# Kernel optimization log

Hardware: AMD Instinct MI355X
Metric: run time of the kernel (lower is better)

Reference implementation:

```python
import jax, jax.numpy as jnp
import numpy as np

B, T, E, H = 256, 1024, 32, 128
N_OBS = 1048576
N_OBS_VOCAB = 11  # n_lands + 2
N_ACT_VOCAB = 5   # n_acts + 2


def setup_inputs() -> dict:
    key = jax.random.key(0)
    ks = jax.random.split(key, 10)
    obs_ids = jax.random.randint(ks[0], (N_OBS,), 0, N_OBS_VOCAB)
    obs_slot = jnp.sort(jax.random.randint(ks[1], (N_OBS,), 0, B * T))
    action_ids = jax.random.randint(ks[2], (B, T), 0, N_ACT_VOCAB)
    is_action = jax.random.bernoulli(ks[3], 0.5, (B, T))
    lengths = jax.random.randint(ks[4], (B,), T // 4, T + 1)
    input_lengths = jnp.sort(lengths)[::-1]  # pack_padded_sequence requires descending
    s = 1.0 / np.sqrt(H)
    action_emb = jax.random.normal(ks[5], (N_ACT_VOCAB, E), jnp.float32)
    obs_emb = jax.random.normal(ks[6], (N_OBS_VOCAB, E), jnp.float32)
    W_ih = jax.random.uniform(ks[7], (4 * H, E), jnp.float32, -s, s)
    W_hh = jax.random.uniform(ks[8], (4 * H, H), jnp.float32, -s, s)
    b_ih = jax.random.uniform(ks[9], (4 * H,), jnp.float32, -s, s)
    b_hh = jnp.zeros((4 * H,), jnp.float32)
    return dict(obs_ids=obs_ids, obs_slot=obs_slot, action_ids=action_ids,
                is_action=is_action, input_lengths=input_lengths,
                action_emb=action_emb, obs_emb=obs_emb,
                W_ih=W_ih, W_hh=W_hh, b_ih=b_ih, b_hh=b_hh)


def _embed(obs_ids, obs_slot, action_ids, is_action, action_emb, obs_emb):
    # fused ragged embedding-bag: gather + segment-sum over observation lists
    obs_sum = jax.ops.segment_sum(obs_emb[obs_ids], obs_slot, num_segments=B * T)
    obs_sum = obs_sum.reshape(B, T, E)
    act = action_emb[action_ids]  # [B,T,E]
    return jnp.where(is_action[..., None], act, obs_sum)


def _lstm(embedded, input_lengths, W_ih, W_hh, b_ih, b_hh):
    mask = (jnp.arange(T)[None, :] < input_lengths[:, None])  # [B,T]
    xs = jnp.swapaxes(embedded, 0, 1)                         # [T,B,E]
    ms = mask.T[..., None].astype(embedded.dtype)             # [T,B,1]

    def step(carry, inp):
        h, c = carry
        x, m = inp
        gates = x @ W_ih.T + h @ W_hh.T + (b_ih + b_hh)  # [B,4H]
        i, f, g, o = jnp.split(gates, 4, axis=-1)        # torch gate order i,f,g,o
        i, f, o = jax.nn.sigmoid(i), jax.nn.sigmoid(f), jax.nn.sigmoid(o)
        g = jnp.tanh(g)
        c_new = f * c + i * g
        h_new = o * jnp.tanh(c_new)
        h = m * h_new + (1.0 - m) * h  # frozen past length (packed semantics)
        c = m * c_new + (1.0 - m) * c
        return (h, c), h * m           # pad_packed zero-pads past length

    h0 = jnp.zeros((B, H), embedded.dtype)
    c0 = jnp.zeros((B, H), embedded.dtype)
    (hN, cN), outs = jax.lax.scan(step, (h0, c0), (xs, ms))
    return jnp.swapaxes(outs, 0, 1), hN[None], cN[None]  # outputs [B,T,H], h/c [1,B,H]


def reference(obs_ids, obs_slot, action_ids, is_action, input_lengths,
              action_emb, obs_emb, W_ih, W_hh, b_ih, b_hh):
    embedded = _embed(obs_ids, obs_slot, action_ids, is_action, action_emb, obs_emb)
    outputs, h, c = _lstm(embedded, input_lengths, W_ih, W_hh, b_ih, b_hh)
    return outputs, h, c, embedded
```

## Files before the change

### kernel.cpp

```cpp
#include <hip/hip_runtime.h>

#define B_ 256
#define T_ 1024
#define E_ 32
#define H_ 128
#define NOBS_ 1048576
#define RPB 4
#define NBLK (B_ / RPB)
#define NW 8
#define THREADS (NW * 64)

#define HROW 144
#define HBUF (RPB * HROW)

#define L2E 1.4426950408889634f

typedef __attribute__((ext_vector_type(8))) short bf16x8;
typedef __attribute__((ext_vector_type(4))) float f32x4;
typedef __attribute__((ext_vector_type(4))) int   i32x4;

#define LDS_BARRIER() asm volatile("s_waitcnt lgkmcnt(0)\n\ts_barrier" ::: "memory")

__device__ __forceinline__ short f2bf(float x) {
    unsigned u = __float_as_uint(x);
    unsigned r = u + 0x7FFFu + ((u >> 16) & 1u);
    return (short)(r >> 16);
}

__global__ void embed_kernel(const int* __restrict__ obs_ids,
                             const int* __restrict__ obs_slot,
                             const int* __restrict__ action_ids,
                             const int* __restrict__ is_action,
                             const float* __restrict__ action_emb,
                             const float* __restrict__ obs_emb,
                             float* __restrict__ embedded) {
    __shared__ float s_act[5 * E_];
    __shared__ float s_obs[11 * E_];
    for (int i = threadIdx.x; i < 5 * E_; i += blockDim.x) s_act[i] = action_emb[i];
    for (int i = threadIdx.x; i < 11 * E_; i += blockDim.x) s_obs[i] = obs_emb[i];
    __syncthreads();

    int s = blockIdx.x * blockDim.x + threadIdx.x;
    if (s >= B_ * T_) return;

    float acc[E_];
    if (is_action[s]) {
        int a = action_ids[s];
        #pragma unroll
        for (int e = 0; e < E_; e++) acc[e] = s_act[a * E_ + e];
    } else {
        #pragma unroll
        for (int e = 0; e < E_; e++) acc[e] = 0.0f;
        int lo = 0, hi = NOBS_;
        while (lo < hi) {
            int mid = (lo + hi) >> 1;
            if (obs_slot[mid] < s) lo = mid + 1; else hi = mid;
        }
        int j = lo;
        while (j < NOBS_ && obs_slot[j] == s) {
            int id = obs_ids[j];
            #pragma unroll
            for (int e = 0; e < E_; e++) acc[e] += s_obs[id * E_ + e];
            j++;
        }
    }
    float4* dst = (float4*)(embedded + (size_t)s * E_);
    #pragma unroll
    for (int q = 0; q < E_ / 4; q++) {
        float4 v; v.x = acc[4*q]; v.y = acc[4*q+1]; v.z = acc[4*q+2]; v.w = acc[4*q+3];
        dst[q] = v;
    }
}

__launch_bounds__(THREADS, 2)
__global__ void lstm_kernel(const float* __restrict__ embedded,
                            const int* __restrict__ lengths,
                            const float* __restrict__ W_ih,
                            const float* __restrict__ W_hh,
                            const float* __restrict__ b_ih,
                            const float* __restrict__ b_hh,
                            float* __restrict__ outputs,
                            float* __restrict__ h_out,
                            float* __restrict__ c_out) {
    __shared__ __align__(16) char h_lds[2 * HBUF];

    const int tid  = threadIdx.x;
    const int lane = tid & 63;
    const int wave = tid >> 6;
    const int row0 = blockIdx.x * RPB;

    const int col16  = (wave << 4) + (lane & 15);
    const int kgrp8  = (lane >> 4) * 8;
    const int kgrp16 = (lane >> 4) * 16;
    const int brow   = (lane & 15) >> 2;
    const int g_own  = lane >> 4;

    bf16x8 wx[4];
    f32x4  biasv[4];
    i32x4  wh[4][2];
    float  dq[4];
    #pragma unroll
    for (int gt = 0; gt < 4; gt++) {
        const float scale = (gt == 2) ? (2.0f * L2E) : L2E;
        const int gcol = gt * H_ + col16;
        {
            const float* p = W_ih + (size_t)gcol * E_ + kgrp8;
            bf16x8 v;
            #pragma unroll
            for (int j = 0; j < 8; j++) v[j] = f2bf(p[j] * scale);
            wx[gt] = v;
        }
        biasv[gt] = (f32x4)((b_ih[gcol] + b_hh[gcol]) * scale);

        const float* q = W_hh + (size_t)gcol * H_;
        float m = 0.0f;
        #pragma unroll
        for (int t2 = 0; t2 < 2; t2++)
            #pragma unroll
            for (int j = 0; j < 16; j++)
                m = fmaxf(m, fabsf(q[t2 * 64 + kgrp16 + j]));
        m = fmaxf(m, __shfl_xor(m, 16));
        m = fmaxf(m, __shfl_xor(m, 32));
        const float s = 127.0f / m;
        dq[gt] = scale * m * (1.0f / (127.0f * 127.0f));
        #pragma unroll
        for (int t2 = 0; t2 < 2; t2++) {
            i32x4 v;
            #pragma unroll
            for (int d = 0; d < 4; d++) {
                int word = 0;
                #pragma unroll
                for (int b2 = 0; b2 < 4; b2++) {
                    int qi = (int)rintf(q[t2 * 64 + kgrp16 + d * 4 + b2] * s);
                    word |= (qi & 0xFF) << (b2 * 8);
                }
                v[d] = word;
            }
            wh[gt][t2] = v;
        }
    }

    const int len = lengths[row0 + g_own];
    float cr = 0.0f, hr = 0.0f;

    const float* xp = embedded + ((size_t)(row0 + brow) * T_) * E_ + kgrp8;

    const int rbase = brow * HROW + kgrp16;
    const int wofs  = g_own * HROW + col16;
    float* const out_base = outputs + (size_t)(row0 + g_own) * T_ * H_ + col16;

    for (int i = tid; i < 2 * HBUF; i += THREADS) h_lds[i] = 0;
    __syncthreads();

    float4 xAlo = *(const float4*)(xp + 0 * E_);
    float4 xAhi = *(const float4*)(xp + 0 * E_ + 4);
    float4 xBlo = *(const float4*)(xp + 1 * E_);
    float4 xBhi = *(const float4*)(xp + 1 * E_ + 4);

    auto step = [&](int t, int RD, int WR, float4& xlo, float4& xhi, bool PF) {
        i32x4 ah0 = *(const i32x4*)&h_lds[RD + rbase + 0 * 64];
        i32x4 ah1 = *(const i32x4*)&h_lds[RD + rbase + 1 * 64];

        int x0, x1, x2, x3;
        asm("v_cvt_pk_bf16_f32 %0, %1, %2" : "=v"(x0) : "v"(xlo.x), "v"(xlo.y));
        asm("v_cvt_pk_bf16_f32 %0, %1, %2" : "=v"(x1) : "v"(xlo.z), "v"(xlo.w));
        asm("v_cvt_pk_bf16_f32 %0, %1, %2" : "=v"(x2) : "v"(xhi.x), "v"(xhi.y));
        asm("v_cvt_pk_bf16_f32 %0, %1, %2" : "=v"(x3) : "v"(xhi.z), "v"(xhi.w));
        i32x4 xi; xi[0] = x0; xi[1] = x1; xi[2] = x2; xi[3] = x3;
        bf16x8 xa = __builtin_bit_cast(bf16x8, xi);

        if (PF) {
            const float* xq = xp + (size_t)(t + 2) * E_;
            xlo = *(const float4*)(xq + 0);
            xhi = *(const float4*)(xq + 4);
        }

        f32x4 accf[4];
        i32x4 acci[4];
        const i32x4 zero = (i32x4)0;
        #pragma unroll
        for (int gt = 0; gt < 4; gt++)
            accf[gt] = __builtin_amdgcn_mfma_f32_16x16x32_bf16(xa, wx[gt], biasv[gt], 0, 0, 0);
        #pragma unroll
        for (int gt = 0; gt < 4; gt++)
            acci[gt] = __builtin_amdgcn_mfma_i32_16x16x64_i8(ah0, wh[gt][0], zero, 0, 0, 0);
        #pragma unroll
        for (int gt = 0; gt < 4; gt++)
            acci[gt] = __builtin_amdgcn_mfma_i32_16x16x64_i8(ah1, wh[gt][1], acci[gt], 0, 0, 0);

        float a_i = fmaf((float)acci[0][0], dq[0], accf[0][0]);
        float a_f = fmaf((float)acci[1][0], dq[1], accf[1][0]);
        float a_g = fmaf((float)acci[2][0], dq[2], accf[2][0]);
        float a_o = fmaf((float)acci[3][0], dq[3], accf[3][0]);

        float Ai = exp2f(-a_i);
        float Eg = exp2f(fminf(a_g, 80.0f));
        float ig = (Eg - 1.0f) * __builtin_amdgcn_rcpf((1.0f + Ai) * (Eg + 1.0f));
        float Af = exp2f(-a_f);
        float f_ = __builtin_amdgcn_rcpf(1.0f + Af);
        float c_new = fmaf(f_, cr, ig);
        float Ec = exp2f(fminf((2.0f * L2E) * c_new, 80.0f));
        float Ao = exp2f(-a_o);
        float h_new = (Ec - 1.0f) * __builtin_amdgcn_rcpf((1.0f + Ao) * (Ec + 1.0f));

        bool m = (t < len);
        cr = m ? c_new : cr;
        hr = m ? h_new : hr;
        out_base[(size_t)t * H_] = m ? h_new : 0.0f;

        int qh = (int)rintf(hr * 127.0f);
        h_lds[WR + wofs] = (char)qh;

        LDS_BARRIER();
    };

    for (int t = 0; t < T_ - 2; t += 2) {
        step(t,     0,    HBUF, xAlo, xAhi, true);
        step(t + 1, HBUF, 0,    xBlo, xBhi, true);
    }
    step(T_ - 2, 0,    HBUF, xAlo, xAhi, false);
    step(T_ - 1, HBUF, 0,    xBlo, xBhi, false);

    h_out[(size_t)(row0 + g_own) * H_ + col16] = hr;
    c_out[(size_t)(row0 + g_own) * H_ + col16] = cr;
}

extern "C" void kernel_launch(void* const* d_in, const int* in_sizes, int n_in,
                              void* d_out, int out_size, void* d_ws, size_t ws_size,
                              hipStream_t stream) {
    const int*   obs_ids       = (const int*)d_in[0];
    const int*   obs_slot      = (const int*)d_in[1];
    const int*   action_ids    = (const int*)d_in[2];
    const int*   is_action     = (const int*)d_in[3];
    const int*   input_lengths = (const int*)d_in[4];
    const float* action_emb    = (const float*)d_in[5];
    const float* obs_emb       = (const float*)d_in[6];
    const float* W_ih          = (const float*)d_in[7];
    const float* W_hh          = (const float*)d_in[8];
    const float* b_ih          = (const float*)d_in[9];
    const float* b_hh          = (const float*)d_in[10];

    float* out      = (float*)d_out;
    float* outputs  = out;
    float* h_out    = out + (size_t)B_ * T_ * H_;
    float* c_out    = h_out + (size_t)B_ * H_;
    float* embedded = c_out + (size_t)B_ * H_;

    hipLaunchKernelGGL(embed_kernel, dim3((B_ * T_ + 255) / 256), dim3(256), 0, stream,
                       obs_ids, obs_slot, action_ids, is_action, action_emb, obs_emb, embedded);

    hipLaunchKernelGGL(lstm_kernel, dim3(NBLK), dim3(THREADS), 0, stream,
                       embedded, input_lengths, W_ih, W_hh, b_ih, b_hh,
                       outputs, h_out, c_out);
}
```

Before: 487.9 us.

## Precompute bf16 inputs in embed kernel and software-pipeline input projection MFMAs

The embed kernel now also writes a bf16 copy of the embeddings into workspace when enough workspace is available, so the LSTM kernel loads one 16-byte vector per step instead of two float4 loads plus conversions. The input-projection MFMAs for step t+1 are issued after the recurrent MFMAs of step t, taking them off the serial h-dependency chain. The cost is an extra bf16 write in the embed kernel and more live accumulator registers, which could hurt occupancy; it falls back to the fp32 path if the workspace is too small.

```diff
diff --git a/kernel.cpp b/kernel.cpp
--- a/kernel.cpp
+++ b/kernel.cpp
@@ -33,7 +33,8 @@
                              const int* __restrict__ is_action,
                              const float* __restrict__ action_emb,
                              const float* __restrict__ obs_emb,
-                             float* __restrict__ embedded) {
+                             float* __restrict__ embedded,
+                             unsigned short* __restrict__ xbf) {
     __shared__ float s_act[5 * E_];
     __shared__ float s_obs[11 * E_];
     for (int i = threadIdx.x; i < 5 * E_; i += blockDim.x) s_act[i] = action_emb[i];
@@ -70,10 +71,20 @@
         float4 v; v.x = acc[4*q]; v.y = acc[4*q+1]; v.z = acc[4*q+2]; v.w = acc[4*q+3];
         dst[q] = v;
     }
+    if (xbf) {
+        unsigned short tmp[E_];
+        #pragma unroll
+        for (int e = 0; e < E_; e++) tmp[e] = (unsigned short)f2bf(acc[e]);
+        int4* d2 = (int4*)(xbf + (size_t)s * E_);
+        #pragma unroll
+        for (int q = 0; q < E_ / 8; q++) d2[q] = ((const int4*)tmp)[q];
+    }
 }
 
+template<bool BF16X>
 __launch_bounds__(THREADS, 2)
 __global__ void lstm_kernel(const float* __restrict__ embedded,
+                            const unsigned short* __restrict__ xbf,
                             const int* __restrict__ lengths,
                             const float* __restrict__ W_ih,
                             const float* __restrict__ W_hh,
@@ -143,7 +154,8 @@
     const int len = lengths[row0 + g_own];
     float cr = 0.0f, hr = 0.0f;
 
-    const float* xp = embedded + ((size_t)(row0 + brow) * T_) * E_ + kgrp8;
+    const unsigned short* xpb = xbf + ((size_t)(row0 + brow) * T_) * E_ + kgrp8;
+    const float*          xpf = embedded + ((size_t)(row0 + brow) * T_) * E_ + kgrp8;
 
     const int rbase = brow * HROW + kgrp16;
     const int wofs  = g_own * HROW + col16;
@@ -152,46 +164,69 @@
     for (int i = tid; i < 2 * HBUF; i += THREADS) h_lds[i] = 0;
     __syncthreads();
 
-    float4 xAlo = *(const float4*)(xp + 0 * E_);
-    float4 xAhi = *(const float4*)(xp + 0 * E_ + 4);
-    float4 xBlo = *(const float4*)(xp + 1 * E_);
-    float4 xBhi = *(const float4*)(xp + 1 * E_ + 4);
-
-    auto step = [&](int t, int RD, int WR, float4& xlo, float4& xhi, bool PF) {
+    int4 xfA, xfB;
+    float4 flA, fhA, flB, fhB;
+    auto loadx = [&](int t, int4& xi4, float4& fl, float4& fh) {
+        if (BF16X) {
+            xi4 = *(const int4*)(xpb + (size_t)t * E_);
+        } else {
+            fl = *(const float4*)(xpf + (size_t)t * E_);
+            fh = *(const float4*)(xpf + (size_t)t * E_ + 4);
+        }
+    };
+    auto mkfrag = [&](const int4& xi4, const float4& fl, const float4& fh) -> bf16x8 {
+        if (BF16X) {
+            return __builtin_bit_cast(bf16x8, xi4);
+        } else {
+            int x0, x1, x2, x3;
+            asm("v_cvt_pk_bf16_f32 %0, %1, %2" : "=v"(x0) : "v"(fl.x), "v"(fl.y));
+            asm("v_cvt_pk_bf16_f32 %0, %1, %2" : "=v"(x1) : "v"(fl.z), "v"(fl.w));
+            asm("v_cvt_pk_bf16_f32 %0, %1, %2" : "=v"(x2) : "v"(fh.x), "v"(fh.y));
+            asm("v_cvt_pk_bf16_f32 %0, %1, %2" : "=v"(x3) : "v"(fh.z), "v"(fh.w));
+            i32x4 xi; xi[0] = x0; xi[1] = x1; xi[2] = x2; xi[3] = x3;
+            return __builtin_bit_cast(bf16x8, xi);
+        }
+    };
+
+    loadx(0, xfA, flA, fhA);
+    loadx(1, xfB, flB, fhB);
+    f32x4 accfA[4], accfB[4];
+    {
+        bf16x8 xa = mkfrag(xfA, flA, fhA);
+        #pragma unroll
+        for (int gt = 0; gt < 4; gt++)
+            accfA[gt] = __builtin_amdgcn_mfma_f32_16x16x32_bf16(xa, wx[gt], biasv[gt], 0, 0, 0);
+    }
+
+    auto step = [&](int t, int RD, int WR,
+                    f32x4* accf_cur, f32x4* accf_nxt,
+                    const int4& xf_nx, const float4& fl_nx, const float4& fh_nx,
+                    int4& xf_pf, float4& fl_pf, float4& fh_pf,
+                    bool PF1, bool PF2) {
         i32x4 ah0 = *(const i32x4*)&h_lds[RD + rbase + 0 * 64];
         i32x4 ah1 = *(const i32x4*)&h_lds[RD + rbase + 1 * 64];
 
-        int x0, x1, x2, x3;
-        asm("v_cvt_pk_bf16_f32 %0, %1, %2" : "=v"(x0) : "v"(xlo.x), "v"(xlo.y));
-        asm("v_cvt_pk_bf16_f32 %0, %1, %2" : "=v"(x1) : "v"(xlo.z), "v"(xlo.w));
-        asm("v_cvt_pk_bf16_f32 %0, %1, %2" : "=v"(x2) : "v"(xhi.x), "v"(xhi.y));
-        asm("v_cvt_pk_bf16_f32 %0, %1, %2" : "=v"(x3) : "v"(xhi.z), "v"(xhi.w));
-        i32x4 xi; xi[0] = x0; xi[1] = x1; xi[2] = x2; xi[3] = x3;
-        bf16x8 xa = __builtin_bit_cast(bf16x8, xi);
-
-        if (PF) {
-            const float* xq = xp + (size_t)(t + 2) * E_;
-            xlo = *(const float4*)(xq + 0);
-            xhi = *(const float4*)(xq + 4);
-        }
-
-        f32x4 accf[4];
         i32x4 acci[4];
         const i32x4 zero = (i32x4)0;
         #pragma unroll
         for (int gt = 0; gt < 4; gt++)
-            accf[gt] = __builtin_amdgcn_mfma_f32_16x16x32_bf16(xa, wx[gt], biasv[gt], 0, 0, 0);
-        #pragma unroll
-        for (int gt = 0; gt < 4; gt++)
             acci[gt] = __builtin_amdgcn_mfma_i32_16x16x64_i8(ah0, wh[gt][0], zero, 0, 0, 0);
         #pragma unroll
         for (int gt = 0; gt < 4; gt++)
             acci[gt] = __builtin_amdgcn_mfma_i32_16x16x64_i8(ah1, wh[gt][1], acci[gt], 0, 0, 0);
 
-        float a_i = fmaf((float)acci[0][0], dq[0], accf[0][0]);
-        float a_f = fmaf((float)acci[1][0], dq[1], accf[1][0]);
-        float a_g = fmaf((float)acci[2][0], dq[2], accf[2][0]);
-        float a_o = fmaf((float)acci[3][0], dq[3], accf[3][0]);
+        if (PF1) {
+            bf16x8 xa = mkfrag(xf_nx, fl_nx, fh_nx);
+            #pragma unroll
+            for (int gt = 0; gt < 4; gt++)
+                accf_nxt[gt] = __builtin_amdgcn_mfma_f32_16x16x32_bf16(xa, wx[gt], biasv[gt], 0, 0, 0);
+        }
+        if (PF2) loadx(t + 2, xf_pf, fl_pf, fh_pf);
+
+        float a_i = fmaf((float)acci[0][0], dq[0], accf_cur[0][0]);
+        float a_f = fmaf((float)acci[1][0], dq[1], accf_cur[1][0]);
+        float a_g = fmaf((float)acci[2][0], dq[2], accf_cur[2][0]);
+        float a_o = fmaf((float)acci[3][0], dq[3], accf_cur[3][0]);
 
         float Ai = exp2f(-a_i);
         float Eg = exp2f(fminf(a_g, 80.0f));
@@ -215,11 +250,11 @@
     };
 
     for (int t = 0; t < T_ - 2; t += 2) {
-        step(t,     0,    HBUF, xAlo, xAhi, true);
-        step(t + 1, HBUF, 0,    xBlo, xBhi, true);
-    }
-    step(T_ - 2, 0,    HBUF, xAlo, xAhi, false);
-    step(T_ - 1, HBUF, 0,    xBlo, xBhi, false);
+        step(t,     0,    HBUF, accfA, accfB, xfB, flB, fhB, xfA, flA, fhA, true, true);
+        step(t + 1, HBUF, 0,    accfB, accfA, xfA, flA, fhA, xfB, flB, fhB, true, t + 3 < T_);
+    }
+    step(T_ - 2, 0,    HBUF, accfA, accfB, xfB, flB, fhB, xfA, flA, fhA, true,  false);
+    step(T_ - 1, HBUF, 0,    accfB, accfA, xfA, flA, fhA, xfB, flB, fhB, false, false);
 
     h_out[(size_t)(row0 + g_own) * H_ + col16] = hr;
     c_out[(size_t)(row0 + g_own) * H_ + col16] = cr;
@@ -246,10 +281,21 @@
     float* c_out    = h_out + (size_t)B_ * H_;
     float* embedded = c_out + (size_t)B_ * H_;
 
+    const size_t xbf_bytes = (size_t)B_ * T_ * E_ * sizeof(unsigned short);
+    const bool use_bf16x = (ws_size >= xbf_bytes);
+    unsigned short* xbf = use_bf16x ? (unsigned short*)d_ws : nullptr;
+
     hipLaunchKernelGGL(embed_kernel, dim3((B_ * T_ + 255) / 256), dim3(256), 0, stream,
-                       obs_ids, obs_slot, action_ids, is_action, action_emb, obs_emb, embedded);
-
-    hipLaunchKernelGGL(lstm_kernel, dim3(NBLK), dim3(THREADS), 0, stream,
-                       embedded, input_lengths, W_ih, W_hh, b_ih, b_hh,
-                       outputs, h_out, c_out);
+                       obs_ids, obs_slot, action_ids, is_action, action_emb, obs_emb,
+                       embedded, xbf);
+
+    if (use_bf16x) {
+        hipLaunchKernelGGL((lstm_kernel<true>), dim3(NBLK), dim3(THREADS), 0, stream,
+                           embedded, xbf, input_lengths, W_ih, W_hh, b_ih, b_hh,
+                           outputs, h_out, c_out);
+    } else {
+        hipLaunchKernelGGL((lstm_kernel<false>), dim3(NBLK), dim3(THREADS), 0, stream,
+                           embedded, xbf, input_lengths, W_ih, W_hh, b_ih, b_hh,
+                           outputs, h_out, c_out);
+    }
 }
```

Measured after the change: 481.5 us. Within noise of the previous version (-1.3%).

## Interleave two independent batch groups per block to overlap MFMA with elementwise

Applied to the files above, without the earlier changes.

Each LSTM block now handles two groups of four sequences (A and B). It staggers their recurrences so one group's matrix multiplies run while the other group's gate elementwise math and stores execute. The embed kernel also writes a bf16 copy of the inputs to workspace, which halves the per-step input load and removes the conversion inside the loop. The gate math is reworked to share one reciprocal across the input and forget gates, with tighter exp clamps. The grid halves to 32 blocks, giving fewer CUs more serial work. A fallback single-group kernel runs when the workspace is too small.

```diff
diff --git a/kernel.cpp b/kernel.cpp
--- a/kernel.cpp
+++ b/kernel.cpp
@@ -5,15 +5,11 @@
 #define E_ 32
 #define H_ 128
 #define NOBS_ 1048576
-#define RPB 4
-#define NBLK (B_ / RPB)
-#define NW 8
-#define THREADS (NW * 64)
+#define L2E 1.4426950408889634f
+#define CLM 30.0f
 
 #define HROW 144
-#define HBUF (RPB * HROW)
-
-#define L2E 1.4426950408889634f
+#define HBUF (4 * HROW)
 
 typedef __attribute__((ext_vector_type(8))) short bf16x8;
 typedef __attribute__((ext_vector_type(4))) float f32x4;
@@ -25,6 +21,16 @@
     unsigned u = __float_as_uint(x);
     unsigned r = u + 0x7FFFu + ((u >> 16) & 1u);
     return (short)(r >> 16);
+}
+
+__device__ __forceinline__ bf16x8 pack8(float4 lo, float4 hi) {
+    int x0, x1, x2, x3;
+    asm("v_cvt_pk_bf16_f32 %0, %1, %2" : "=v"(x0) : "v"(lo.x), "v"(lo.y));
+    asm("v_cvt_pk_bf16_f32 %0, %1, %2" : "=v"(x1) : "v"(lo.z), "v"(lo.w));
+    asm("v_cvt_pk_bf16_f32 %0, %1, %2" : "=v"(x2) : "v"(hi.x), "v"(hi.y));
+    asm("v_cvt_pk_bf16_f32 %0, %1, %2" : "=v"(x3) : "v"(hi.z), "v"(hi.w));
+    i32x4 xi; xi[0] = x0; xi[1] = x1; xi[2] = x2; xi[3] = x3;
+    return __builtin_bit_cast(bf16x8, xi);
 }
 
 __global__ void embed_kernel(const int* __restrict__ obs_ids,
@@ -33,7 +39,8 @@
                              const int* __restrict__ is_action,
                              const float* __restrict__ action_emb,
                              const float* __restrict__ obs_emb,
-                             float* __restrict__ embedded) {
+                             float* __restrict__ embedded,
+                             unsigned short* __restrict__ xbf) {
     __shared__ float s_act[5 * E_];
     __shared__ float s_obs[11 * E_];
     for (int i = threadIdx.x; i < 5 * E_; i += blockDim.x) s_act[i] = action_emb[i];
@@ -70,24 +77,33 @@
         float4 v; v.x = acc[4*q]; v.y = acc[4*q+1]; v.z = acc[4*q+2]; v.w = acc[4*q+3];
         dst[q] = v;
     }
-}
-
-__launch_bounds__(THREADS, 2)
-__global__ void lstm_kernel(const float* __restrict__ embedded,
-                            const int* __restrict__ lengths,
-                            const float* __restrict__ W_ih,
-                            const float* __restrict__ W_hh,
-                            const float* __restrict__ b_ih,
-                            const float* __restrict__ b_hh,
-                            float* __restrict__ outputs,
-                            float* __restrict__ h_out,
-                            float* __restrict__ c_out) {
-    __shared__ __align__(16) char h_lds[2 * HBUF];
+    if (xbf) {
+        unsigned short tmp[E_];
+        #pragma unroll
+        for (int e = 0; e < E_; e++) tmp[e] = (unsigned short)f2bf(acc[e]);
+        int4* d2 = (int4*)(xbf + (size_t)s * E_);
+        #pragma unroll
+        for (int q = 0; q < E_ / 8; q++) d2[q] = ((const int4*)tmp)[q];
+    }
+}
+
+__launch_bounds__(512, 2)
+__global__ void lstm_ap2_kernel(const unsigned short* __restrict__ xbf,
+                                const int* __restrict__ lengths,
+                                const float* __restrict__ W_ih,
+                                const float* __restrict__ W_hh,
+                                const float* __restrict__ b_ih,
+                                const float* __restrict__ b_hh,
+                                float* __restrict__ outputs,
+                                float* __restrict__ h_out,
+                                float* __restrict__ c_out) {
+    __shared__ __align__(16) char ldsA[HBUF];
+    __shared__ __align__(16) char ldsB[HBUF];
 
     const int tid  = threadIdx.x;
     const int lane = tid & 63;
     const int wave = tid >> 6;
-    const int row0 = blockIdx.x * RPB;
+    const int row0 = blockIdx.x * 8;
 
     const int col16  = (wave << 4) + (lane & 15);
     const int kgrp8  = (lane >> 4) * 8;
@@ -95,10 +111,7 @@
     const int brow   = (lane & 15) >> 2;
     const int g_own  = lane >> 4;
 
-    bf16x8 wx[4];
-    f32x4  biasv[4];
-    i32x4  wh[4][2];
-    float  dq[4];
+    bf16x8 wx[4]; f32x4 biasv[4]; i32x4 wh[4][2]; float dq[4];
     #pragma unroll
     for (int gt = 0; gt < 4; gt++) {
         const float scale = (gt == 2) ? (2.0f * L2E) : L2E;
@@ -111,7 +124,6 @@
             wx[gt] = v;
         }
         biasv[gt] = (f32x4)((b_ih[gcol] + b_hh[gcol]) * scale);
-
         const float* q = W_hh + (size_t)gcol * H_;
         float m = 0.0f;
         #pragma unroll
@@ -140,87 +152,211 @@
         }
     }
 
+    const int lenA = lengths[row0 + g_own];
+    const int lenB = lengths[row0 + 4 + g_own];
+    float cA = 0.f, hA = 0.f, cB = 0.f, hB = 0.f;
+
+    const int rbase = brow * HROW + kgrp16;
+    const int wofs  = g_own * HROW + col16;
+
+    const unsigned short* xpA = xbf + ((size_t)(row0 + brow) * T_) * E_ + kgrp8;
+    const unsigned short* xpB = xbf + ((size_t)(row0 + 4 + brow) * T_) * E_ + kgrp8;
+    float* const outA = outputs + (size_t)(row0 + g_own) * T_ * H_ + col16;
+    float* const outB = outputs + (size_t)(row0 + 4 + g_own) * T_ * H_ + col16;
+
+    for (int i = tid; i < HBUF; i += 512) { ldsA[i] = 0; ldsB[i] = 0; }
+    __syncthreads();
+
+    int4 xA = *(const int4*)xpA;
+    int4 xB = *(const int4*)xpB;
+
+    i32x4 accA[4] = {}, accB[4] = {};
+    f32x4 accfA[4] = {}, accfB[4] = {};
+
+    auto EW = [&](const i32x4* acc, const f32x4* accf, int t, int len,
+                  float& cr, float& hr, float* outp, char* ldsw) {
+        float a_i = fmaf((float)acc[0][0], dq[0], accf[0][0]);
+        float a_f = fmaf((float)acc[1][0], dq[1], accf[1][0]);
+        float a_g = fmaf((float)acc[2][0], dq[2], accf[2][0]);
+        float a_o = fmaf((float)acc[3][0], dq[3], accf[3][0]);
+        float Ai = exp2f(fminf(-a_i, CLM));
+        float Af = exp2f(fminf(-a_f, CLM));
+        float Eg = exp2f(fminf(a_g, CLM));
+        float pAi = 1.0f + Ai, pAf = 1.0f + Af, pEg = Eg + 1.0f;
+        float D  = pAi * pEg;
+        float R  = __builtin_amdgcn_rcpf(D * pAf);
+        float f_ = D * R;
+        float ig = (Eg - 1.0f) * pAf * R;
+        float c_new = fmaf(f_, cr, ig);
+        float Ec = exp2f(fminf(c_new * (2.0f * L2E), CLM));
+        float Ao = exp2f(fminf(-a_o, CLM));
+        float Rh = __builtin_amdgcn_rcpf((1.0f + Ao) * (Ec + 1.0f));
+        float h_new = (Ec - 1.0f) * Rh;
+        bool m = (t < len);
+        cr = m ? c_new : cr;
+        hr = m ? h_new : hr;
+        outp[(size_t)t * H_] = m ? h_new : 0.0f;
+        int qh = (int)rintf(hr * 127.0f);
+        ldsw[wofs] = (char)qh;
+    };
+
+    for (int i = 0; i < T_; ++i) {
+        i32x4 a0 = *(const i32x4*)&ldsA[rbase];
+        i32x4 a1 = *(const i32x4*)&ldsA[rbase + 64];
+        bf16x8 xaA = __builtin_bit_cast(bf16x8, xA);
+        if (i + 1 < T_) xA = *(const int4*)(xpA + (size_t)(i + 1) * E_);
+        #pragma unroll
+        for (int gt = 0; gt < 4; gt++)
+            accfA[gt] = __builtin_amdgcn_mfma_f32_16x16x32_bf16(xaA, wx[gt], biasv[gt], 0, 0, 0);
+        #pragma unroll
+        for (int gt = 0; gt < 4; gt++)
+            accA[gt] = __builtin_amdgcn_mfma_i32_16x16x64_i8(a0, wh[gt][0], (i32x4)0, 0, 0, 0);
+        #pragma unroll
+        for (int gt = 0; gt < 4; gt++)
+            accA[gt] = __builtin_amdgcn_mfma_i32_16x16x64_i8(a1, wh[gt][1], accA[gt], 0, 0, 0);
+        if (i > 0) EW(accB, accfB, i - 1, lenB, cB, hB, outB, ldsB);
+        LDS_BARRIER();
+
+        i32x4 b0 = *(const i32x4*)&ldsB[rbase];
+        i32x4 b1 = *(const i32x4*)&ldsB[rbase + 64];
+        bf16x8 xaB = __builtin_bit_cast(bf16x8, xB);
+        if (i + 1 < T_) xB = *(const int4*)(xpB + (size_t)(i + 1) * E_);
+        #pragma unroll
+        for (int gt = 0; gt < 4; gt++)
+            accfB[gt] = __builtin_amdgcn_mfma_f32_16x16x32_bf16(xaB, wx[gt], biasv[gt], 0, 0, 0);
+        #pragma unroll
+        for (int gt = 0; gt < 4; gt++)
+            accB[gt] = __builtin_amdgcn_mfma_i32_16x16x64_i8(b0, wh[gt][0], (i32x4)0, 0, 0, 0);
+        #pragma unroll
+        for (int gt = 0; gt < 4; gt++)
+            accB[gt] = __builtin_amdgcn_mfma_i32_16x16x64_i8(b1, wh[gt][1], accB[gt], 0, 0, 0);
+        EW(accA, accfA, i, lenA, cA, hA, outA, ldsA);
+        LDS_BARRIER();
+    }
+    EW(accB, accfB, T_ - 1, lenB, cB, hB, outB, ldsB);
+
+    h_out[(size_t)(row0 + g_own) * H_ + col16] = hA;
+    c_out[(size_t)(row0 + g_own) * H_ + col16] = cA;
+    h_out[(size_t)(row0 + 4 + g_own) * H_ + col16] = hB;
+    c_out[(size_t)(row0 + 4 + g_own) * H_ + col16] = cB;
+}
+
+__launch_bounds__(512, 2)
+__global__ void lstm_fb_kernel(const float* __restrict__ embedded,
+                               const int* __restrict__ lengths,
+                               const float* __restrict__ W_ih,
+                               const float* __restrict__ W_hh,
+                               const float* __restrict__ b_ih,
+                               const float* __restrict__ b_hh,
+                               float* __restrict__ outputs,
+                               float* __restrict__ h_out,
+                               float* __restrict__ c_out) {
+    __shared__ __align__(16) char h_lds[2 * HBUF];
+    const int tid  = threadIdx.x;
+    const int lane = tid & 63;
+    const int wave = tid >> 6;
+    const int row0 = blockIdx.x * 4;
+    const int col16  = (wave << 4) + (lane & 15);
+    const int kgrp8  = (lane >> 4) * 8;
+    const int kgrp16 = (lane >> 4) * 16;
+    const int brow   = (lane & 15) >> 2;
+    const int g_own  = lane >> 4;
+
+    bf16x8 wx[4]; f32x4 biasv[4]; i32x4 wh[4][2]; float dq[4];
+    #pragma unroll
+    for (int gt = 0; gt < 4; gt++) {
+        const float scale = (gt == 2) ? (2.0f * L2E) : L2E;
+        const int gcol = gt * H_ + col16;
+        {
+            const float* p = W_ih + (size_t)gcol * E_ + kgrp8;
+            bf16x8 v;
+            #pragma unroll
+            for (int j = 0; j < 8; j++) v[j] = f2bf(p[j] * scale);
+            wx[gt] = v;
+        }
+        biasv[gt] = (f32x4)((b_ih[gcol] + b_hh[gcol]) * scale);
+        const float* q = W_hh + (size_t)gcol * H_;
+        float m = 0.0f;
+        #pragma unroll
+        for (int t2 = 0; t2 < 2; t2++)
+            #pragma unroll
+            for (int j = 0; j < 16; j++)
+                m = fmaxf(m, fabsf(q[t2 * 64 + kgrp16 + j]));
+        m = fmaxf(m, __shfl_xor(m, 16));
+        m = fmaxf(m, __shfl_xor(m, 32));
+        const float s = 127.0f / m;
+        dq[gt] = scale * m * (1.0f / (127.0f * 127.0f));
+        #pragma unroll
+        for (int t2 = 0; t2 < 2; t2++) {
+            i32x4 v;
+            #pragma unroll
+            for (int d = 0; d < 4; d++) {
+                int word = 0;
+                #pragma unroll
+                for (int b2 = 0; b2 < 4; b2++) {
+                    int qi = (int)rintf(q[t2 * 64 + kgrp16 + d * 4 + b2] * s);
+                    word |= (qi & 0xFF) << (b2 * 8);
+                }
+                v[d] = word;
+            }
+            wh[gt][t2] = v;
+        }
+    }
     const int len = lengths[row0 + g_own];
     float cr = 0.0f, hr = 0.0f;
-
     const float* xp = embedded + ((size_t)(row0 + brow) * T_) * E_ + kgrp8;
-
     const int rbase = brow * HROW + kgrp16;
     const int wofs  = g_own * HROW + col16;
     float* const out_base = outputs + (size_t)(row0 + g_own) * T_ * H_ + col16;
-
-    for (int i = tid; i < 2 * HBUF; i += THREADS) h_lds[i] = 0;
+    for (int i = tid; i < 2 * HBUF; i += 512) h_lds[i] = 0;
     __syncthreads();
-
-    float4 xAlo = *(const float4*)(xp + 0 * E_);
-    float4 xAhi = *(const float4*)(xp + 0 * E_ + 4);
-    float4 xBlo = *(const float4*)(xp + 1 * E_);
-    float4 xBhi = *(const float4*)(xp + 1 * E_ + 4);
-
-    auto step = [&](int t, int RD, int WR, float4& xlo, float4& xhi, bool PF) {
-        i32x4 ah0 = *(const i32x4*)&h_lds[RD + rbase + 0 * 64];
-        i32x4 ah1 = *(const i32x4*)&h_lds[RD + rbase + 1 * 64];
-
-        int x0, x1, x2, x3;
-        asm("v_cvt_pk_bf16_f32 %0, %1, %2" : "=v"(x0) : "v"(xlo.x), "v"(xlo.y));
-        asm("v_cvt_pk_bf16_f32 %0, %1, %2" : "=v"(x1) : "v"(xlo.z), "v"(xlo.w));
-        asm("v_cvt_pk_bf16_f32 %0, %1, %2" : "=v"(x2) : "v"(xhi.x), "v"(xhi.y));
-        asm("v_cvt_pk_bf16_f32 %0, %1, %2" : "=v"(x3) : "v"(xhi.z), "v"(xhi.w));
-        i32x4 xi; xi[0] = x0; xi[1] = x1; xi[2] = x2; xi[3] = x3;
-        bf16x8 xa = __builtin_bit_cast(bf16x8, xi);
-
-        if (PF) {
-            const float* xq = xp + (size_t)(t + 2) * E_;
-            xlo = *(const float4*)(xq + 0);
-            xhi = *(const float4*)(xq + 4);
-        }
-
-        f32x4 accf[4];
-        i32x4 acci[4];
-        const i32x4 zero = (i32x4)0;
+    float4 xlo = *(const float4*)xp, xhi = *(const float4*)(xp + 4);
+    int RD = 0;
+    for (int t = 0; t < T_; ++t) {
+        i32x4 ah0 = *(const i32x4*)&h_lds[RD + rbase];
+        i32x4 ah1 = *(const i32x4*)&h_lds[RD + rbase + 64];
+        bf16x8 xa = pack8(xlo, xhi);
+        if (t + 1 < T_) {
+            const float* xq = xp + (size_t)(t + 1) * E_;
+            xlo = *(const float4*)xq; xhi = *(const float4*)(xq + 4);
+        }
+        f32x4 accf[4]; i32x4 acci[4];
         #pragma unroll
         for (int gt = 0; gt < 4; gt++)
             accf[gt] = __builtin_amdgcn_mfma_f32_16x16x32_bf16(xa, wx[gt], biasv[gt], 0, 0, 0);
         #pragma unroll
         for (int gt = 0; gt < 4; gt++)
-            acci[gt] = __builtin_amdgcn_mfma_i32_16x16x64_i8(ah0, wh[gt][0], zero, 0, 0, 0);
+            acci[gt] = __builtin_amdgcn_mfma_i32_16x16x64_i8(ah0, wh[gt][0], (i32x4)0, 0, 0, 0);
         #pragma unroll
         for (int gt = 0; gt < 4; gt++)
             acci[gt] = __builtin_amdgcn_mfma_i32_16x16x64_i8(ah1, wh[gt][1], acci[gt], 0, 0, 0);
-
         float a_i = fmaf((float)acci[0][0], dq[0], accf[0][0]);
         float a_f = fmaf((float)acci[1][0], dq[1], accf[1][0]);
         float a_g = fmaf((float)acci[2][0], dq[2], accf[2][0]);
         float a_o = fmaf((float)acci[3][0], dq[3], accf[3][0]);
-
-        float Ai = exp2f(-a_i);
-        float Eg = exp2f(fminf(a_g, 80.0f));
-        float ig = (Eg - 1.0f) * __builtin_amdgcn_rcpf((1.0f + Ai) * (Eg + 1.0f));
-        float Af = exp2f(-a_f);
-        float f_ = __builtin_amdgcn_rcpf(1.0f + Af);
+        float Ai = exp2f(fminf(-a_i, CLM));
+        float Af = exp2f(fminf(-a_f, CLM));
+        float Eg = exp2f(fminf(a_g, CLM));
+        float pAi = 1.0f + Ai, pAf = 1.0f + Af, pEg = Eg + 1.0f;
+        float D = pAi * pEg;
+        float R = __builtin_amdgcn_rcpf(D * pAf);
+        float f_ = D * R;
+        float ig = (Eg - 1.0f) * pAf * R;
         float c_new = fmaf(f_, cr, ig);
-        float Ec = exp2f(fminf((2.0f * L2E) * c_new, 80.0f));
-        float Ao = exp2f(-a_o);
-        float h_new = (Ec - 1.0f) * __builtin_amdgcn_rcpf((1.0f + Ao) * (Ec + 1.0f));
-
+        float Ec = exp2f(fminf(c_new * (2.0f * L2E), CLM));
+        float Ao = exp2f(fminf(-a_o, CLM));
+        float Rh = __builtin_amdgcn_rcpf((1.0f + Ao) * (Ec + 1.0f));
+        float h_new = (Ec - 1.0f) * Rh;
         bool m = (t < len);
         cr = m ? c_new : cr;
         hr = m ? h_new : hr;
         out_base[(size_t)t * H_] = m ? h_new : 0.0f;
-
         int qh = (int)rintf(hr * 127.0f);
+        const int WR = RD ^ (2 * HBUF / 2);
         h_lds[WR + wofs] = (char)qh;
-
+        RD = WR;
         LDS_BARRIER();
-    };
-
-    for (int t = 0; t < T_ - 2; t += 2) {
-        step(t,     0,    HBUF, xAlo, xAhi, true);
-        step(t + 1, HBUF, 0,    xBlo, xBhi, true);
-    }
-    step(T_ - 2, 0,    HBUF, xAlo, xAhi, false);
-    step(T_ - 1, HBUF, 0,    xBlo, xBhi, false);
-
+    }
     h_out[(size_t)(row0 + g_own) * H_ + col16] = hr;
     c_out[(size_t)(row0 + g_own) * H_ + col16] = cr;
 }
@@ -246,10 +382,21 @@
     float* c_out    = h_out + (size_t)B_ * H_;
     float* embedded = c_out + (size_t)B_ * H_;
 
+    const size_t xbf_bytes = (size_t)B_ * T_ * E_ * sizeof(unsigned short);
+    const bool use_ap = (ws_size >= xbf_bytes);
+    unsigned short* xbf = use_ap ? (unsigned short*)d_ws : nullptr;
+
     hipLaunchKernelGGL(embed_kernel, dim3((B_ * T_ + 255) / 256), dim3(256), 0, stream,
-                       obs_ids, obs_slot, action_ids, is_action, action_emb, obs_emb, embedded);
-
-    hipLaunchKernelGGL(lstm_kernel, dim3(NBLK), dim3(THREADS), 0, stream,
-                       embedded, input_lengths, W_ih, W_hh, b_ih, b_hh,
-                       outputs, h_out, c_out);
-}
+                       obs_ids, obs_slot, action_ids, is_action, action_emb, obs_emb,
+                       embedded, xbf);
+
+    if (use_ap) {
+        hipLaunchKernelGGL(lstm_ap2_kernel, dim3(B_ / 8), dim3(512), 0, stream,
+                           xbf, input_lengths, W_ih, W_hh, b_ih, b_hh,
+                           outputs, h_out, c_out);
+    } else {
+        hipLaunchKernelGGL(lstm_fb_kernel, dim3(B_ / 4), dim3(512), 0, stream,
+                           embedded, input_lengths, W_ih, W_hh, b_ih, b_hh,
+                           outputs, h_out, c_out);
+    }
+}
```

Measured after the change: 937.8 us. +92.2%, slower.
